# Kernel tuning notes

Measured on AMD Instinct MI355X. Metric: run time of the kernel, lower is better.

Reference implementation:

```python
import jax, jax.numpy as jnp
from jax import lax
import numpy as np

B, C, H, W = 8, 16, 128, 128
HID = 128


def setup_inputs() -> dict:
    key = jax.random.key(0)
    k1, k2, k3 = jax.random.split(key, 3)
    x = jax.random.uniform(k1, (B, C, H, W), dtype=jnp.float32)
    # fc1: Conv2d(3*C, HID, 1); fc2: Conv2d(HID, C, 1). Original zero-inits fc2;
    # we use small random weights so the dynamics (and grads) are non-trivial.
    w1 = jax.random.normal(k2, (HID, 3 * C), dtype=jnp.float32) * (1.0 / jnp.sqrt(3.0 * C))
    b1 = jnp.zeros((HID,), jnp.float32)
    w2 = jax.random.normal(k3, (C, HID), dtype=jnp.float32) * 0.02
    b2 = jnp.zeros((C,), jnp.float32)
    return {"x": x, "w1": w1, "b1": b1, "w2": w2, "b2": b2, "n_steps": 16}


def _dw_conv(x, k3x3):
    # depthwise 3x3 conv, same kernel for every channel, padding=1
    kern = jnp.broadcast_to(k3x3, (C, 1, 3, 3))
    return lax.conv_general_dilated(
        x, kern, window_strides=(1, 1), padding="SAME",
        feature_group_count=C,
        dimension_numbers=("NCHW", "OIHW", "NCHW"))


def _ca_step(out, step_key, w1, b1, w2, b2, sobel_x, sobel_y):
    sx = _dw_conv(out, sobel_x)
    sy = _dw_conv(out, sobel_y)
    ident = out  # identity 3x3 kernel == identity map
    perception = jnp.concatenate([ident, sx, sy], axis=1)  # [B,3C,H,W]
    h = jnp.einsum("bchw,oc->bohw", perception, w1) + b1[None, :, None, None]
    h = jax.nn.relu(h)
    diff = jnp.einsum("bchw,oc->bohw", h, w2) + b2[None, :, None, None]
    # stochastic per-pixel update mask, broadcast over channels
    mask = (jax.random.uniform(step_key, (B, 1, H, W)) < 0.5).astype(out.dtype)
    new = out + diff * mask
    # alive gate: 3x3 maxpool on alpha channel (index 3) > 0.1
    alpha = new[:, 3:4]
    pooled = lax.reduce_window(alpha, -jnp.inf, lax.max,
                               (1, 1, 3, 3), (1, 1, 1, 1), "SAME")
    alive = (pooled > 0.1).astype(new.dtype)
    return new * alive


def reference(x, w1, b1, w2, b2, n_steps):
    keys = jax.random.split(jax.random.key(42), n_steps)
    def body(out, k):
        return _ca_step(out, k, w1, b1, w2, b2, _SOBEL_X, _SOBEL_Y), None
    out, _ = lax.scan(body, x, keys)
    return out

_SOBEL_Y = jnp.array([[1.0, 2.0, 1.0], [0.0, 0.0, 0.0], [-1.0, -2.0, -1.0]],
                     dtype=jnp.float32) / 8.0
_SOBEL_X = _SOBEL_Y.T
```

## Files before the change

kernel.cpp:

```cpp
#include <hip/hip_runtime.h>
#include <stdint.h>

#define BB 8
#define CC 16
#define HH_ 128
#define WW 128
#define HIDN 128
#define HWSZ (HH_ * WW)
#define NPIX (BB * HWSZ)
#define NSTEPS 16

__host__ __device__ inline void threefry2x32(uint32_t k0, uint32_t k1,
                                             uint32_t x0, uint32_t x1,
                                             uint32_t* o0, uint32_t* o1) {
  uint32_t ks[3] = {k0, k1, k0 ^ k1 ^ 0x1BD11BDAu};
  const uint32_t rots[2][4] = {{13u, 15u, 26u, 6u}, {17u, 29u, 16u, 24u}};
  x0 += ks[0];
  x1 += ks[1];
#pragma unroll
  for (int g = 0; g < 5; ++g) {
    const uint32_t* r = rots[g & 1];
#pragma unroll
    for (int i = 0; i < 4; ++i) {
      x0 += x1;
      x1 = (x1 << r[i]) | (x1 >> (32u - r[i]));
      x1 ^= x0;
    }
    x0 += ks[(g + 1) % 3];
    x1 += ks[(g + 2) % 3] + (uint32_t)(g + 1);
  }
  *o0 = x0;
  *o1 = x1;
}

__device__ __forceinline__ float jax_mask_bit(uint32_t key0, uint32_t key1, int g) {
  uint32_t t0, t1;
  threefry2x32(key0, key1, 0u, (uint32_t)g, &t0, &t1);
  uint32_t bits = t0 ^ t1;
  float u = __uint_as_float((bits >> 9) | 0x3f800000u) - 1.0f;
  return (u < 0.5f) ? 1.0f : 0.0f;
}

__global__ __launch_bounds__(256, 2) void ca_step_mlp(
    const float* __restrict__ cur, const float* __restrict__ w1,
    const float* __restrict__ b1, const float* __restrict__ w2,
    const float* __restrict__ b2, float* __restrict__ nxt,
    uint32_t key0, uint32_t key1) {
  __shared__ float lw2t[HIDN * CC];

  for (int i = threadIdx.x; i < HIDN * CC; i += 256) {
    int hh = i >> 4, o = i & 15;
    lw2t[i] = w2[o * HIDN + hh];
  }
  __syncthreads();

  const int g = blockIdx.x * 256 + threadIdx.x;
  const int b = g >> 14;
  const int hw = g & (HWSZ - 1);
  const int h = hw >> 7;
  const int w = hw & (WW - 1);

  const bool hu = h > 0, hd = h < HH_ - 1, wl = w > 0, wr = w < WW - 1;
  const int du = hu ? -WW : 0;
  const int dd = hd ? WW : 0;
  const int dl = wl ? -1 : 0;
  const int dr = wr ? 1 : 0;

  const float* xb = cur + (size_t)b * CC * HWSZ + hw;

  float p[48];
#pragma unroll
  for (int c = 0; c < CC; ++c) {
    const float* xc = xb + c * HWSZ;
    float n00 = xc[du + dl]; if (!(hu && wl)) n00 = 0.f;
    float n01 = xc[du];      if (!hu)         n01 = 0.f;
    float n02 = xc[du + dr]; if (!(hu && wr)) n02 = 0.f;
    float n10 = xc[dl];      if (!wl)         n10 = 0.f;
    float n11 = xc[0];
    float n12 = xc[dr];      if (!wr)         n12 = 0.f;
    float n20 = xc[dd + dl]; if (!(hd && wl)) n20 = 0.f;
    float n21 = xc[dd];      if (!hd)         n21 = 0.f;
    float n22 = xc[dd + dr]; if (!(hd && wr)) n22 = 0.f;
    p[c] = n11;
    p[16 + c] = (n00 - n02 + 2.f * (n10 - n12) + n20 - n22) * 0.125f;
    p[32 + c] = (n00 + 2.f * n01 + n02 - n20 - 2.f * n21 - n22) * 0.125f;
  }

  float diff[CC];
#pragma unroll
  for (int o = 0; o < CC; ++o) diff[o] = b2[o];

  for (int ph = 0; ph < 8; ++ph) {
    __syncthreads();
#pragma unroll
    for (int j = 0; j < 16; ++j) {
      const int hh = ph * 16 + j;
      const float4* wrow = (const float4*)(w1 + hh * 48);
      float a0 = b1[hh], a1 = 0.f, a2 = 0.f, a3 = 0.f;
#pragma unroll
      for (int q = 0; q < 3; ++q) {
        float4 w0 = wrow[q * 4 + 0];
        float4 w1v = wrow[q * 4 + 1];
        float4 w2v = wrow[q * 4 + 2];
        float4 w3 = wrow[q * 4 + 3];
        const int base = q * 16;
        a0 = fmaf(w0.x, p[base + 0], a0);
        a0 = fmaf(w0.y, p[base + 1], a0);
        a0 = fmaf(w0.z, p[base + 2], a0);
        a0 = fmaf(w0.w, p[base + 3], a0);
        a1 = fmaf(w1v.x, p[base + 4], a1);
        a1 = fmaf(w1v.y, p[base + 5], a1);
        a1 = fmaf(w1v.z, p[base + 6], a1);
        a1 = fmaf(w1v.w, p[base + 7], a1);
        a2 = fmaf(w2v.x, p[base + 8], a2);
        a2 = fmaf(w2v.y, p[base + 9], a2);
        a2 = fmaf(w2v.z, p[base + 10], a2);
        a2 = fmaf(w2v.w, p[base + 11], a2);
        a3 = fmaf(w3.x, p[base + 12], a3);
        a3 = fmaf(w3.y, p[base + 13], a3);
        a3 = fmaf(w3.z, p[base + 14], a3);
        a3 = fmaf(w3.w, p[base + 15], a3);
      }
      float acc = (a0 + a1) + (a2 + a3);
      acc = fmaxf(acc, 0.f);
      const float4* w2r = (const float4*)(lw2t + hh * CC);
#pragma unroll
      for (int o4 = 0; o4 < 4; ++o4) {
        float4 wv = w2r[o4];
        diff[o4 * 4 + 0] = fmaf(wv.x, acc, diff[o4 * 4 + 0]);
        diff[o4 * 4 + 1] = fmaf(wv.y, acc, diff[o4 * 4 + 1]);
        diff[o4 * 4 + 2] = fmaf(wv.z, acc, diff[o4 * 4 + 2]);
        diff[o4 * 4 + 3] = fmaf(wv.w, acc, diff[o4 * 4 + 3]);
      }
    }
  }

  const float m = jax_mask_bit(key0, key1, g);

  float* nb = nxt + (size_t)b * CC * HWSZ + hw;
#pragma unroll
  for (int c = 0; c < CC; ++c) {
    nb[c * HWSZ] = fmaf(diff[c], m, p[c]);
  }
}

__global__ __launch_bounds__(256) void ca_step_alive(
    const float* __restrict__ nw, float* __restrict__ out) {
  const int g = blockIdx.x * 256 + threadIdx.x;
  const int b = g >> 14;
  const int hw = g & (HWSZ - 1);
  const int h = hw >> 7;
  const int w = hw & (WW - 1);
  const bool hu = h > 0, hd = h < HH_ - 1, wl = w > 0, wr = w < WW - 1;

  const float* ab = nw + ((size_t)b * CC + 3) * HWSZ + hw;
  float pooled = ab[0];
  if (hu) {
    pooled = fmaxf(pooled, ab[-WW]);
    if (wl) pooled = fmaxf(pooled, ab[-WW - 1]);
    if (wr) pooled = fmaxf(pooled, ab[-WW + 1]);
  }
  if (hd) {
    pooled = fmaxf(pooled, ab[WW]);
    if (wl) pooled = fmaxf(pooled, ab[WW - 1]);
    if (wr) pooled = fmaxf(pooled, ab[WW + 1]);
  }
  if (wl) pooled = fmaxf(pooled, ab[-1]);
  if (wr) pooled = fmaxf(pooled, ab[1]);

  const float alive = (pooled > 0.1f) ? 1.0f : 0.0f;

  const float* nb = nw + (size_t)b * CC * HWSZ + hw;
  float* ob = out + (size_t)b * CC * HWSZ + hw;
#pragma unroll
  for (int c = 0; c < CC; ++c) ob[c * HWSZ] = nb[c * HWSZ] * alive;
}

extern "C" void kernel_launch(void* const* d_in, const int* in_sizes, int n_in,
                              void* d_out, int out_size, void* d_ws,
                              size_t ws_size, hipStream_t stream) {
  const float* x = (const float*)d_in[0];
  const float* w1 = (const float*)d_in[1];
  const float* b1 = (const float*)d_in[2];
  const float* w2 = (const float*)d_in[3];
  const float* b2 = (const float*)d_in[4];

  float* out = (float*)d_out;
  float* nbuf = (float*)d_ws;

  uint32_t k0s[NSTEPS], k1s[NSTEPS];
  for (int s = 0; s < NSTEPS; ++s)
    threefry2x32(0u, 42u, 0u, (uint32_t)s, &k0s[s], &k1s[s]);

  dim3 grid(NPIX / 256), block(256);
  for (int s = 0; s < NSTEPS; ++s) {
    const float* src = (s == 0) ? x : out;
    ca_step_mlp<<<grid, block, 0, stream>>>(src, w1, b1, w2, b2, nbuf,
                                            k0s[s], k1s[s]);
    ca_step_alive<<<grid, block, 0, stream>>>(nbuf, out);
  }
}
```

Baseline: 993.4 us.

## Stage fc1 sobel weights in LDS with double-buffered prefetch, batch fc2 per chunk

Moves the sobel-part of the fc1 weights (32 of 48 columns per hidden unit) into shared memory. Each row is prefetched into registers one hidden unit ahead, ping-ponging between two buffers. The identity-part weights and fc2 weights now come straight from global, uniform across the block. fc2 accumulation runs once per 16-hidden chunk over a hacc array, replacing a per-hidden LDS broadcast, and the per-chunk syncthreads is dropped. The extra live registers (two 8-float4 buffers plus 16 hidden values) risk spills or lower occupancy under launch_bounds(256,2).

After: 893.6 us. -10.1%, faster.

```diff
diff --git a/kernel.cpp b/kernel.cpp
--- a/kernel.cpp
+++ b/kernel.cpp
@@ -41,16 +41,22 @@
   return (u < 0.5f) ? 1.0f : 0.0f;
 }
 
+#define FMA4(acc, wv, pp, k)          \
+  acc = fmaf(wv.x, pp[(k) + 0], acc); \
+  acc = fmaf(wv.y, pp[(k) + 1], acc); \
+  acc = fmaf(wv.z, pp[(k) + 2], acc); \
+  acc = fmaf(wv.w, pp[(k) + 3], acc);
+
 __global__ __launch_bounds__(256, 2) void ca_step_mlp(
     const float* __restrict__ cur, const float* __restrict__ w1,
     const float* __restrict__ b1, const float* __restrict__ w2,
     const float* __restrict__ b2, float* __restrict__ nxt,
     uint32_t key0, uint32_t key1) {
-  __shared__ float lw2t[HIDN * CC];
-
-  for (int i = threadIdx.x; i < HIDN * CC; i += 256) {
-    int hh = i >> 4, o = i & 15;
-    lw2t[i] = w2[o * HIDN + hh];
+  __shared__ float lw1hi[HIDN * 32];
+
+  for (int i = threadIdx.x; i < HIDN * 8; i += 256) {
+    int hh = i >> 3, q = i & 7;
+    ((float4*)lw1hi)[i] = ((const float4*)(w1 + hh * 48 + 16))[q];
   }
   __syncthreads();
 
@@ -90,48 +96,62 @@
 #pragma unroll
   for (int o = 0; o < CC; ++o) diff[o] = b2[o];
 
-  for (int ph = 0; ph < 8; ++ph) {
-    __syncthreads();
+  const float4* lw = (const float4*)lw1hi;
+  float4 bufA[8], bufB[8];
+#pragma unroll
+  for (int q = 0; q < 8; ++q) bufA[q] = lw[q];
+
+  float hacc[16];
+
+  for (int chunk = 0; chunk < 8; ++chunk) {
 #pragma unroll
     for (int j = 0; j < 16; ++j) {
-      const int hh = ph * 16 + j;
-      const float4* wrow = (const float4*)(w1 + hh * 48);
+      const int hh = chunk * 16 + j;
+      const int hnx = (hh + 1) & 127;
+      float4* pb = (j & 1) ? bufA : bufB;
+      const float4* cb = (j & 1) ? bufB : bufA;
+#pragma unroll
+      for (int q = 0; q < 8; ++q) pb[q] = lw[hnx * 8 + q];
+
+      const float4* wlo = (const float4*)(w1 + hh * 48);
+      float4 l0 = wlo[0], l1 = wlo[1], l2 = wlo[2], l3 = wlo[3];
       float a0 = b1[hh], a1 = 0.f, a2 = 0.f, a3 = 0.f;
-#pragma unroll
-      for (int q = 0; q < 3; ++q) {
-        float4 w0 = wrow[q * 4 + 0];
-        float4 w1v = wrow[q * 4 + 1];
-        float4 w2v = wrow[q * 4 + 2];
-        float4 w3 = wrow[q * 4 + 3];
-        const int base = q * 16;
-        a0 = fmaf(w0.x, p[base + 0], a0);
-        a0 = fmaf(w0.y, p[base + 1], a0);
-        a0 = fmaf(w0.z, p[base + 2], a0);
-        a0 = fmaf(w0.w, p[base + 3], a0);
-        a1 = fmaf(w1v.x, p[base + 4], a1);
-        a1 = fmaf(w1v.y, p[base + 5], a1);
-        a1 = fmaf(w1v.z, p[base + 6], a1);
-        a1 = fmaf(w1v.w, p[base + 7], a1);
-        a2 = fmaf(w2v.x, p[base + 8], a2);
-        a2 = fmaf(w2v.y, p[base + 9], a2);
-        a2 = fmaf(w2v.z, p[base + 10], a2);
-        a2 = fmaf(w2v.w, p[base + 11], a2);
-        a3 = fmaf(w3.x, p[base + 12], a3);
-        a3 = fmaf(w3.y, p[base + 13], a3);
-        a3 = fmaf(w3.z, p[base + 14], a3);
-        a3 = fmaf(w3.w, p[base + 15], a3);
-      }
-      float acc = (a0 + a1) + (a2 + a3);
-      acc = fmaxf(acc, 0.f);
-      const float4* w2r = (const float4*)(lw2t + hh * CC);
-#pragma unroll
-      for (int o4 = 0; o4 < 4; ++o4) {
-        float4 wv = w2r[o4];
-        diff[o4 * 4 + 0] = fmaf(wv.x, acc, diff[o4 * 4 + 0]);
-        diff[o4 * 4 + 1] = fmaf(wv.y, acc, diff[o4 * 4 + 1]);
-        diff[o4 * 4 + 2] = fmaf(wv.z, acc, diff[o4 * 4 + 2]);
-        diff[o4 * 4 + 3] = fmaf(wv.w, acc, diff[o4 * 4 + 3]);
-      }
+      FMA4(a0, l0, p, 0)
+      FMA4(a1, l1, p, 4)
+      FMA4(a2, l2, p, 8)
+      FMA4(a3, l3, p, 12)
+      FMA4(a0, cb[0], p, 16)
+      FMA4(a1, cb[1], p, 20)
+      FMA4(a2, cb[2], p, 24)
+      FMA4(a3, cb[3], p, 28)
+      FMA4(a0, cb[4], p, 32)
+      FMA4(a1, cb[5], p, 36)
+      FMA4(a2, cb[6], p, 40)
+      FMA4(a3, cb[7], p, 44)
+      hacc[j] = fmaxf((a0 + a1) + (a2 + a3), 0.f);
+    }
+#pragma unroll
+    for (int o = 0; o < CC; ++o) {
+      const float4* w2r = (const float4*)(w2 + o * HIDN + chunk * 16);
+      float4 u0 = w2r[0], u1 = w2r[1], u2 = w2r[2], u3 = w2r[3];
+      float d = diff[o];
+      d = fmaf(u0.x, hacc[0], d);
+      d = fmaf(u0.y, hacc[1], d);
+      d = fmaf(u0.z, hacc[2], d);
+      d = fmaf(u0.w, hacc[3], d);
+      d = fmaf(u1.x, hacc[4], d);
+      d = fmaf(u1.y, hacc[5], d);
+      d = fmaf(u1.z, hacc[6], d);
+      d = fmaf(u1.w, hacc[7], d);
+      d = fmaf(u2.x, hacc[8], d);
+      d = fmaf(u2.y, hacc[9], d);
+      d = fmaf(u2.z, hacc[10], d);
+      d = fmaf(u2.w, hacc[11], d);
+      d = fmaf(u3.x, hacc[12], d);
+      d = fmaf(u3.y, hacc[13], d);
+      d = fmaf(u3.z, hacc[14], d);
+      d = fmaf(u3.w, hacc[15], d);
+      diff[o] = d;
     }
   }
 
```
